# Optimization experiments

Measured on AMD Instinct MI355X. Metric: run time of the kernel, lower is better.

The kernel has to match this reference:

```python
import jax, jax.numpy as jnp
import numpy as np
import math

# Model dims (from VisionMamba defaults)
D = 768        # embed_dim
DI = 1536      # d_inner = 2*D
N = 16         # d_state
R = 48         # dt_rank = ceil(D/16)
K = 4          # d_conv
DEPTH = 24
B = 4
H, W, P, CIN = 1280, 960, 64, 3
GH, GW = H // P, W // P
NPATCH = GH * GW           # 300
L = NPATCH + 1             # 301 with cls token
POS = NPATCH // 2          # middle cls token position = 150
NCLS = 1000
EPS = 1e-5


def setup_inputs() -> dict:
    key = jax.random.key(0)
    c = [0]
    def nk():
        c[0] += 1
        return jax.random.fold_in(key, c[0])
    def rn(shape, s=0.02):
        return jax.random.normal(nk(), shape, jnp.float32) * s
    inp = {}
    inp['img'] = jax.random.normal(nk(), (B, CIN, H, W), jnp.float32)
    inp['patch_w'] = rn((D, CIN, P, P))
    inp['patch_b'] = jnp.zeros((D,), jnp.float32)
    inp['cls_token'] = rn((1, 1, D))
    inp['pos_embed'] = rn((1, L, D))
    inp['norm_w'] = jnp.ones((DEPTH, D), jnp.float32)
    inp['in_proj_w'] = rn((DEPTH, 2 * DI, D))
    for s in ('f', 'b'):
        inp[f'conv_{s}_w'] = rn((DEPTH, DI, K), 0.1)
        inp[f'conv_{s}_b'] = jnp.zeros((DEPTH, DI), jnp.float32)
        inp[f'xproj_{s}_w'] = rn((DEPTH, R + 2 * N, DI))
        inp[f'dt_{s}_w'] = rn((DEPTH, DI, R), 0.1)
        dtv = jnp.exp(jax.random.uniform(nk(), (DEPTH, DI), jnp.float32,
                                         math.log(1e-3), math.log(1e-1)))
        inp[f'dt_{s}_b'] = jnp.log(jnp.expm1(dtv))  # softplus-inverse init
        inp[f'A_{s}_log'] = jnp.broadcast_to(
            jnp.log(jnp.arange(1, N + 1, dtype=jnp.float32)), (DEPTH, DI, N)) + 0.0
        inp[f'D_{s}'] = jnp.ones((DEPTH, DI), jnp.float32)
    inp['out_proj_w'] = rn((DEPTH, D, DI))
    inp['norm_f_w'] = jnp.ones((D,), jnp.float32)
    inp['head_w'] = rn((NCLS, D))
    inp['head_b'] = jnp.zeros((NCLS,), jnp.float32)
    return inp


def _rms(x, w):
    return x * jax.lax.rsqrt(jnp.mean(x * x, axis=-1, keepdims=True) + EPS) * w


def _silu(x):
    return x * jax.nn.sigmoid(x)


def _cconv(x, w, b):
    # depthwise causal conv1d, x: [B,L,DI], w: [DI,K]
    Lx = x.shape[1]
    xp = jnp.pad(x, ((0, 0), (K - 1, 0), (0, 0)))
    return sum(xp[:, k:k + Lx, :] * w[:, k] for k in range(K)) + b


def _ssm(xc, z, xproj_w, dt_w, dt_b, A_log, Dp):
    # selective scan; xc, z: [B,L,DI]
    dbl = jnp.einsum('bld,ed->ble', xc, xproj_w)        # [B,L,R+2N]
    dt_r, Bm, Cm = dbl[..., :R], dbl[..., R:R + N], dbl[..., R + N:]
    dt = jax.nn.softplus(jnp.einsum('blr,dr->bld', dt_r, dt_w) + dt_b)
    A = -jnp.exp(A_log)                                 # [DI,N]
    dA = jnp.exp(dt[..., None] * A)                     # [B,L,DI,N]
    dBu = (dt * xc)[..., None] * Bm[:, :, None, :]      # [B,L,DI,N]
    def step(h, ab):
        a, bu = ab
        h = a * h + bu
        return h, h
    h0 = jnp.zeros((dA.shape[0], DI, N), dA.dtype)
    _, hs = jax.lax.scan(step, h0, (jnp.swapaxes(dA, 0, 1), jnp.swapaxes(dBu, 0, 1)))
    y = jnp.einsum('lbdn,bln->bld', hs, Cm) + xc * Dp
    return y * _silu(z)


def _mixer(h, p):
    (in_w, cfw, cfb, xfw, dtfw, dtfb, Afl, Df,
     cbw, cbb, xbw, dtbw, dtbb, Abl, Db, ow) = p
    xz = jnp.einsum('bld,ed->ble', h, in_w)
    x, z = xz[..., :DI], xz[..., DI:]
    yf = _ssm(_silu(_cconv(x, cfw, cfb)), z, xfw, dtfw, dtfb, Afl, Df)
    xr, zr = x[:, ::-1], z[:, ::-1]
    yb = _ssm(_silu(_cconv(xr, cbw, cbb)), zr, xbw, dtbw, dtbb, Abl, Db)
    y = (yf + yb[:, ::-1]) * 0.5   # bimamba v2 with if_divide_out=True
    return jnp.einsum('ble,de->bld', y, ow)


def _forward(img, patch_w, patch_b, cls_token, pos_embed, norm_w, in_proj_w,
             conv_f_w, conv_f_b, xproj_f_w, dt_f_w, dt_f_b, A_f_log, D_f,
             conv_b_w, conv_b_b, xproj_b_w, dt_b_w, dt_b_b, A_b_log, D_b,
             out_proj_w, norm_f_w, head_w, head_b):
    Bn = img.shape[0]
    # non-overlapping conv patch embed (kernel == stride == 64)
    x = img.reshape(Bn, CIN, GH, P, GW, P)
    x = jnp.einsum('bcipjq,dcpq->bijd', x, patch_w).reshape(Bn, NPATCH, D) + patch_b
    cls = jnp.broadcast_to(cls_token, (Bn, 1, D))
    x = jnp.concatenate([x[:, :POS], cls, x[:, POS:]], axis=1) + pos_embed
    layer_params = (norm_w, in_proj_w, conv_f_w, conv_f_b, xproj_f_w, dt_f_w,
                    dt_f_b, A_f_log, D_f, conv_b_w, conv_b_b, xproj_b_w,
                    dt_b_w, dt_b_b, A_b_log, D_b, out_proj_w)
    def layer(carry, p):
        h, res = carry
        res = res + h                # fused add-norm: Add -> RMSNorm -> Mixer
        hn = _rms(res, p[0])
        h2 = _mixer(hn, p[1:])
        return (h2, res), None
    (h, res), _ = jax.lax.scan(layer, (x, jnp.zeros_like(x)), layer_params)
    out = _rms(res + h, norm_f_w)
    return jnp.einsum('bd,cd->bc', out[:, POS], head_w) + head_b


def reference(img, patch_w, patch_b, cls_token, pos_embed, norm_w, in_proj_w,
              conv_f_w, conv_f_b, xproj_f_w, dt_f_w, dt_f_b, A_f_log, D_f,
              conv_b_w, conv_b_b, xproj_b_w, dt_b_w, dt_b_b, A_b_log, D_b,
              out_proj_w, norm_f_w, head_w, head_b):
    return _forward(img, patch_w, patch_b, cls_token, pos_embed, norm_w,
                    in_proj_w, conv_f_w, conv_f_b, xproj_f_w, dt_f_w, dt_f_b,
                    A_f_log, D_f, conv_b_w, conv_b_b, xproj_b_w, dt_b_w,
                    dt_b_b, A_b_log, D_b, out_proj_w, norm_f_w, head_w, head_b)
```

## Files before the change

kernel.cpp:

```cpp
#include <hip/hip_runtime.h>
#include <hip/hip_bf16.h>
#include <math.h>

#define B_ 4
#define L_ 301
#define D_ 768
#define DI_ 1536
#define NP_ 300
#define POS_ 150
#define M_ 1204
#define SCHUNK 64

typedef __bf16 bf16;
typedef __attribute__((ext_vector_type(8))) __bf16 bf16x8;
typedef __attribute__((ext_vector_type(4))) float floatx4;

__device__ __forceinline__ float siluf(float x) { return x / (1.f + __expf(-x)); }
__device__ __forceinline__ float softplusf(float x) { return x > 20.f ? x : log1pf(__expf(x)); }

__global__ __launch_bounds__(256) void gemm_mfma(
    const bf16* __restrict__ A0, const bf16* __restrict__ A1, int lda,
    const float* __restrict__ W0, const float* __restrict__ W1, int ldw,
    const float* __restrict__ bias0, const float* __restrict__ bias1,
    float* __restrict__ C0, float* __restrict__ C1,
    bf16* __restrict__ Cb0, bf16* __restrict__ Cb1, int ldc,
    int M, int Nw, int Kw, int Ksteps, int act)
{
    const int zz = blockIdx.z;
    const bf16* A = zz ? A1 : A0;
    const float* W = zz ? W1 : W0;
    const float* bias = zz ? bias1 : bias0;
    float* C = zz ? C1 : C0;
    bf16* Cb = zz ? Cb1 : Cb0;

    __shared__ bf16 As[128 * 32];
    __shared__ bf16 Ws[128 * 32];
    const int t = threadIdx.x;
    const int bm = blockIdx.y * 128;
    const int bn = blockIdx.x * 128;
    const int lane = t & 63;
    const int wid = t >> 6;
    const int wr = wid >> 1, wc = wid & 1;
    const int ar = t >> 2;
    const int ac = (t & 3) * 8;

    const bool fullNK = ((Nw & 127) == 0) && ((Kw & 31) == 0);

    floatx4 acc[4][4] = {};

    for (int ks = 0; ks < Ksteps; ks++) {
        const int k0 = ks * 32;
#pragma unroll
        for (int c2 = 0; c2 < 2; c2++) {
            int r = ar + c2 * 64;
            int gm = bm + r; if (gm >= M) gm = M - 1;
            const bf16* gp = A + (size_t)gm * lda + k0 + ac;
            __builtin_amdgcn_global_load_lds(
                (const __attribute__((address_space(1))) void*)gp,
                (__attribute__((address_space(3))) void*)(As + r * 32 + ac),
                16, 0, 0);
        }
#pragma unroll
        for (int c2 = 0; c2 < 2; c2++) {
            int r = ar + c2 * 64;
            int gn = bn + r;
            float vv[8];
            if (fullNK) {
                const floatx4* wp4 = (const floatx4*)(W + (size_t)gn * ldw + k0 + ac);
                floatx4 a4 = wp4[0], b4 = wp4[1];
#pragma unroll
                for (int e = 0; e < 4; e++) { vv[e] = a4[e]; vv[e + 4] = b4[e]; }
            } else {
                const float* wp = W + (size_t)gn * ldw + k0 + ac;
#pragma unroll
                for (int e = 0; e < 8; e++) {
                    int kk = k0 + ac + e;
                    vv[e] = (gn < Nw && kk < Kw) ? wp[e] : 0.f;
                }
            }
            bf16x8 pk;
#pragma unroll
            for (int e = 0; e < 8; e++) pk[e] = (bf16)vv[e];
            *(bf16x8*)(Ws + r * 32 + ac) = pk;
        }
        __syncthreads();
        const int ra = wr * 64 + (lane & 15);
        const int rb = wc * 64 + (lane & 15);
        const int kb = (lane >> 4) * 8;
        bf16x8 af[4], bfm[4];
#pragma unroll
        for (int i = 0; i < 4; i++)
            af[i] = *(const bf16x8*)(As + (ra + i * 16) * 32 + kb);
#pragma unroll
        for (int j = 0; j < 4; j++)
            bfm[j] = *(const bf16x8*)(Ws + (rb + j * 16) * 32 + kb);
#pragma unroll
        for (int i = 0; i < 4; i++)
#pragma unroll
            for (int j = 0; j < 4; j++)
                acc[i][j] = __builtin_amdgcn_mfma_f32_16x16x32_bf16(af[i], bfm[j], acc[i][j], 0, 0, 0);
        __syncthreads();
    }
#pragma unroll
    for (int i = 0; i < 4; i++) {
#pragma unroll
        for (int j = 0; j < 4; j++) {
            int n = bn + wc * 64 + j * 16 + (lane & 15);
            if (n >= Nw) continue;
            float bv = (act >= 1) ? bias[n] : 0.f;
#pragma unroll
            for (int r = 0; r < 4; r++) {
                int m = bm + wr * 64 + i * 16 + (lane >> 4) * 4 + r;
                if (m >= M) continue;
                float v = acc[i][j][r] + bv;
                if (act == 2) v = softplusf(v);
                C[(size_t)m * ldc + n] = v;
                if (Cb) Cb[(size_t)m * ldc + n] = (bf16)v;
            }
        }
    }
}

__global__ __launch_bounds__(256) void gemm_mfma_sk(
    const bf16* __restrict__ A0, const bf16* __restrict__ A1, int lda,
    const float* __restrict__ W0, const float* __restrict__ W1, int ldw,
    float* __restrict__ Cp, size_t chunkStride, int ldc,
    int M, int Nw, int KstepsPer, int SK)
{
    const int z = blockIdx.z;
    const int dir = z / SK;
    const int chunk = z % SK;
    const bf16* A = dir ? A1 : A0;
    const float* W = dir ? W1 : W0;
    float* C = Cp + (size_t)z * chunkStride;

    __shared__ bf16 As[128 * 32];
    __shared__ bf16 Ws[128 * 32];
    const int t = threadIdx.x;
    const int bm = blockIdx.y * 128;
    const int bn = blockIdx.x * 128;
    const int lane = t & 63;
    const int wid = t >> 6;
    const int wr = wid >> 1, wc = wid & 1;
    const int ar = t >> 2;
    const int ac = (t & 3) * 8;

    floatx4 acc[4][4] = {};

    for (int ks = 0; ks < KstepsPer; ks++) {
        const int k0 = (chunk * KstepsPer + ks) * 32;
#pragma unroll
        for (int c2 = 0; c2 < 2; c2++) {
            int r = ar + c2 * 64;
            int gm = bm + r; if (gm >= M) gm = M - 1;
            const bf16* gp = A + (size_t)gm * lda + k0 + ac;
            __builtin_amdgcn_global_load_lds(
                (const __attribute__((address_space(1))) void*)gp,
                (__attribute__((address_space(3))) void*)(As + r * 32 + ac),
                16, 0, 0);
        }
#pragma unroll
        for (int c2 = 0; c2 < 2; c2++) {
            int r = ar + c2 * 64;
            int gn = bn + r;
            bf16x8 pk;
            if (gn < Nw) {
                const floatx4* wp4 = (const floatx4*)(W + (size_t)gn * ldw + k0 + ac);
                floatx4 a4 = wp4[0], b4 = wp4[1];
#pragma unroll
                for (int e = 0; e < 4; e++) { pk[e] = (bf16)a4[e]; pk[e + 4] = (bf16)b4[e]; }
            } else {
#pragma unroll
                for (int e = 0; e < 8; e++) pk[e] = (bf16)0.f;
            }
            *(bf16x8*)(Ws + r * 32 + ac) = pk;
        }
        __syncthreads();
        const int ra = wr * 64 + (lane & 15);
        const int rb = wc * 64 + (lane & 15);
        const int kb = (lane >> 4) * 8;
        bf16x8 af[4], bfm[4];
#pragma unroll
        for (int i = 0; i < 4; i++)
            af[i] = *(const bf16x8*)(As + (ra + i * 16) * 32 + kb);
#pragma unroll
        for (int j = 0; j < 4; j++)
            bfm[j] = *(const bf16x8*)(Ws + (rb + j * 16) * 32 + kb);
#pragma unroll
        for (int i = 0; i < 4; i++)
#pragma unroll
            for (int j = 0; j < 4; j++)
                acc[i][j] = __builtin_amdgcn_mfma_f32_16x16x32_bf16(af[i], bfm[j], acc[i][j], 0, 0, 0);
        __syncthreads();
    }
#pragma unroll
    for (int i = 0; i < 4; i++) {
#pragma unroll
        for (int j = 0; j < 4; j++) {
            int n = bn + wc * 64 + j * 16 + (lane & 15);
            if (n >= Nw) continue;
#pragma unroll
            for (int r = 0; r < 4; r++) {
                int m = bm + wr * 64 + i * 16 + (lane >> 4) * 4 + r;
                if (m >= M) continue;
                C[(size_t)m * ldc + n] = acc[i][j][r];
            }
        }
    }
}

__global__ __launch_bounds__(256) void gemm_mfma_avg_sk(
    const bf16* __restrict__ Af, const bf16* __restrict__ Ab, int lda,
    const float* __restrict__ W, int ldw,
    float* __restrict__ Cp, size_t chunkStride, int ldc,
    int M, int Nw, int KstepsPer, int SK)
{
    const int chunk = blockIdx.z;
    float* C = Cp + (size_t)chunk * chunkStride;

    __shared__ bf16 As[128 * 32];
    __shared__ bf16 Ws[128 * 32];
    const int t = threadIdx.x;
    const int bm = blockIdx.y * 128;
    const int bn = blockIdx.x * 128;
    const int lane = t & 63;
    const int wid = t >> 6;
    const int wr = wid >> 1, wc = wid & 1;
    const int ar = t >> 2;
    const int ac = (t & 3) * 8;

    floatx4 acc[4][4] = {};

    for (int ks = 0; ks < KstepsPer; ks++) {
        const int k0 = (chunk * KstepsPer + ks) * 32;
#pragma unroll
        for (int c2 = 0; c2 < 2; c2++) {
            int r = ar + c2 * 64;
            int gm = bm + r; if (gm >= M) gm = M - 1;
            bf16x8 a8 = *(const bf16x8*)(Af + (size_t)gm * lda + k0 + ac);
            bf16x8 b8 = *(const bf16x8*)(Ab + (size_t)gm * lda + k0 + ac);
            bf16x8 pk;
#pragma unroll
            for (int e = 0; e < 8; e++)
                pk[e] = (bf16)(0.5f * ((float)a8[e] + (float)b8[e]));
            *(bf16x8*)(As + r * 32 + ac) = pk;
        }
#pragma unroll
        for (int c2 = 0; c2 < 2; c2++) {
            int r = ar + c2 * 64;
            int gn = bn + r;
            const floatx4* wp4 = (const floatx4*)(W + (size_t)gn * ldw + k0 + ac);
            floatx4 a4 = wp4[0], b4 = wp4[1];
            bf16x8 pk;
#pragma unroll
            for (int e = 0; e < 4; e++) { pk[e] = (bf16)a4[e]; pk[e + 4] = (bf16)b4[e]; }
            *(bf16x8*)(Ws + r * 32 + ac) = pk;
        }
        __syncthreads();
        const int ra = wr * 64 + (lane & 15);
        const int rb = wc * 64 + (lane & 15);
        const int kb = (lane >> 4) * 8;
        bf16x8 af[4], bfm[4];
#pragma unroll
        for (int i = 0; i < 4; i++)
            af[i] = *(const bf16x8*)(As + (ra + i * 16) * 32 + kb);
#pragma unroll
        for (int j = 0; j < 4; j++)
            bfm[j] = *(const bf16x8*)(Ws + (rb + j * 16) * 32 + kb);
#pragma unroll
        for (int i = 0; i < 4; i++)
#pragma unroll
            for (int j = 0; j < 4; j++)
                acc[i][j] = __builtin_amdgcn_mfma_f32_16x16x32_bf16(af[i], bfm[j], acc[i][j], 0, 0, 0);
        __syncthreads();
    }
#pragma unroll
    for (int i = 0; i < 4; i++) {
#pragma unroll
        for (int j = 0; j < 4; j++) {
            int n = bn + wc * 64 + j * 16 + (lane & 15);
            if (n >= Nw) continue;
#pragma unroll
            for (int r = 0; r < 4; r++) {
                int m = bm + wr * 64 + i * 16 + (lane >> 4) * 4 + r;
                if (m >= M) continue;
                C[(size_t)m * ldc + n] = acc[i][j][r];
            }
        }
    }
}

__global__ void reduce_sk2(const float* __restrict__ Cp, size_t chunkStride, int SK,
                           const float* __restrict__ bias0,
                           float* __restrict__ C0, float* __restrict__ C1,
                           bf16* __restrict__ Cb0, bf16* __restrict__ Cb1,
                           int total, int ldn, int act)
{
    const int dir = blockIdx.y;
    const float* P = Cp + (size_t)dir * SK * chunkStride;
    float* C = dir ? C1 : C0;
    bf16* Cb = dir ? Cb1 : Cb0;
    int idx = blockIdx.x * 256 + threadIdx.x;
    if (idx >= total) return;
    float s = 0.f;
    for (int c = 0; c < SK; c++) s += P[(size_t)c * chunkStride + idx];
    if (act >= 1) s += bias0[idx % ldn];
    if (act == 2) s = softplusf(s);
    C[idx] = s;
    if (Cb) Cb[idx] = (bf16)s;
}

__global__ __launch_bounds__(256) void gemm_patch_mfma(
    const float* __restrict__ img, const float* __restrict__ W,
    float* __restrict__ Cp)
{
    __shared__ bf16 As[128 * 32];
    __shared__ bf16 Ws[128 * 32];
    const int t = threadIdx.x;
    const int bm = blockIdx.y * 128;
    const int bn = blockIdx.x * 128;
    const int chunk = blockIdx.z;
    const int lane = t & 63;
    const int wid = t >> 6;
    const int wr = wid >> 1, wc = wid & 1;
    const int ar = t >> 2;
    const int ac = (t & 3) * 8;
    const int M = 1200, ldw = 12288, ldc = 768;
    float* C = Cp + (size_t)chunk * M * ldc;

    const float* abase[2];
#pragma unroll
    for (int c2 = 0; c2 < 2; c2++) {
        int gm = bm + ar + c2 * 64; if (gm >= M) gm = M - 1;
        int b = gm / 300, rem = gm % 300;
        int gi = rem / 15, gj = rem % 15;
        abase[c2] = img + ((size_t)(b * 3) * 1280 + gi * 64) * 960 + gj * 64;
    }

    floatx4 acc[4][4] = {};

    for (int ks = 0; ks < 48; ks++) {
        const int k0 = (chunk * 48 + ks) * 32;
        const int k = k0 + ac;
        const int q = k & 63, p = (k >> 6) & 63, c = k >> 12;
#pragma unroll
        for (int c2 = 0; c2 < 2; c2++) {
            int r = ar + c2 * 64;
            const float* ip = abase[c2] + ((size_t)c * 1280 + p) * 960 + q;
            const floatx4* ip4 = (const floatx4*)ip;
            floatx4 a4 = ip4[0], b4 = ip4[1];
            bf16x8 pk;
#pragma unroll
            for (int e = 0; e < 4; e++) { pk[e] = (bf16)a4[e]; pk[e + 4] = (bf16)b4[e]; }
            *(bf16x8*)(As + r * 32 + ac) = pk;
        }
#pragma unroll
        for (int c2 = 0; c2 < 2; c2++) {
            int r = ar + c2 * 64;
            int gn = bn + r;
            const floatx4* wp4 = (const floatx4*)(W + (size_t)gn * ldw + k);
            floatx4 a4 = wp4[0], b4 = wp4[1];
            bf16x8 pk;
#pragma unroll
            for (int e = 0; e < 4; e++) { pk[e] = (bf16)a4[e]; pk[e + 4] = (bf16)b4[e]; }
            *(bf16x8*)(Ws + r * 32 + ac) = pk;
        }
        __syncthreads();
        const int ra = wr * 64 + (lane & 15);
        const int rb = wc * 64 + (lane & 15);
        const int kb = (lane >> 4) * 8;
        bf16x8 af[4], bfm[4];
#pragma unroll
        for (int i = 0; i < 4; i++)
            af[i] = *(const bf16x8*)(As + (ra + i * 16) * 32 + kb);
#pragma unroll
        for (int j = 0; j < 4; j++)
            bfm[j] = *(const bf16x8*)(Ws + (rb + j * 16) * 32 + kb);
#pragma unroll
        for (int i = 0; i < 4; i++)
#pragma unroll
            for (int j = 0; j < 4; j++)
                acc[i][j] = __builtin_amdgcn_mfma_f32_16x16x32_bf16(af[i], bfm[j], acc[i][j], 0, 0, 0);
        __syncthreads();
    }
#pragma unroll
    for (int i = 0; i < 4; i++) {
#pragma unroll
        for (int j = 0; j < 4; j++) {
            int n = bn + wc * 64 + j * 16 + (lane & 15);
#pragma unroll
            for (int r = 0; r < 4; r++) {
                int m = bm + wr * 64 + i * 16 + (lane >> 4) * 4 + r;
                if (m >= M) continue;
                C[(size_t)m * ldc + n] = acc[i][j][r];
            }
        }
    }
}

__global__ void gemm_bt(const float* __restrict__ A, int lda,
                        const float* __restrict__ W, int ldw,
                        const float* __restrict__ bias,
                        float* __restrict__ C, int ldc,
                        int M, int N, int K, int act) {
    __shared__ float As[16][68];
    __shared__ float Ws[16][68];
    const int tid = threadIdx.x;
    const int bm = blockIdx.y * 64;
    const int bn = blockIdx.x * 64;
    const int tx = tid & 15, ty = tid >> 4;
    float acc[4][4] = {};
    const int lk = tid & 15;
    const int lm = tid >> 4;
    for (int k0 = 0; k0 < K; k0 += 16) {
        const int ak = k0 + lk;
#pragma unroll
        for (int i = 0; i < 4; i++) {
            int m = bm + lm + i * 16;
            float v = 0.f;
            if (m < M && ak < K) v = A[(long)m * lda + ak];
            As[lk][lm + i * 16] = v;
        }
#pragma unroll
        for (int i = 0; i < 4; i++) {
            int n = bn + lm + i * 16;
            float v = 0.f;
            if (n < N && ak < K) v = W[(long)n * ldw + ak];
            Ws[lk][lm + i * 16] = v;
        }
        __syncthreads();
#pragma unroll
        for (int kk = 0; kk < 16; kk++) {
            float a[4], w[4];
#pragma unroll
            for (int i = 0; i < 4; i++) a[i] = As[kk][ty * 4 + i];
#pragma unroll
            for (int j = 0; j < 4; j++) w[j] = Ws[kk][tx * 4 + j];
#pragma unroll
            for (int i = 0; i < 4; i++)
#pragma unroll
                for (int j = 0; j < 4; j++) acc[i][j] += a[i] * w[j];
        }
        __syncthreads();
    }
#pragma unroll
    for (int i = 0; i < 4; i++) {
        int m = bm + ty * 4 + i;
        if (m >= M) continue;
#pragma unroll
        for (int j = 0; j < 4; j++) {
            int n = bn + tx * 4 + j;
            if (n >= N) continue;
            float v = acc[i][j];
            if (act >= 1) v += bias[n];
            C[(long)m * ldc + n] = v;
        }
    }
}

__global__ void assemble(const float* __restrict__ xt, const float* __restrict__ cls,
                         const float* __restrict__ pos, float* __restrict__ x,
                         float* __restrict__ res) {
    int idx = blockIdx.x * 256 + threadIdx.x;
    if (idx >= B_ * L_ * D_) return;
    int d = idx % D_;
    int l = (idx / D_) % L_;
    int b = idx / (D_ * L_);
    float v;
    if (l == POS_) {
        v = cls[d];
    } else {
        int p = (l < POS_) ? l : l - 1;
        v = xt[((long)b * NP_ + p) * D_ + d];
    }
    x[idx] = v + pos[l * D_ + d];
    res[idx] = 0.f;
}

__global__ void add_rms(float* __restrict__ res, const float* __restrict__ h,
                        const float* __restrict__ w, bf16* __restrict__ hn) {
    int row = blockIdx.x;
    float* rr = res + (long)row * D_;
    const float* hr = h + (long)row * D_;
    float v[3];
    float ss = 0.f;
#pragma unroll
    for (int i = 0; i < 3; i++) {
        int d = threadIdx.x + i * 256;
        float t = rr[d] + hr[d];
        v[i] = t;
        ss += t * t;
    }
#pragma unroll
    for (int off = 1; off < 64; off <<= 1) ss += __shfl_xor(ss, off);
    __shared__ float red[4];
    __shared__ float inv;
    if ((threadIdx.x & 63) == 0) red[threadIdx.x >> 6] = ss;
    __syncthreads();
    if (threadIdx.x == 0) {
        float s = red[0] + red[1] + red[2] + red[3];
        inv = rsqrtf(s / (float)D_ + 1e-5f);
    }
    __syncthreads();
    float iv = inv;
#pragma unroll
    for (int i = 0; i < 3; i++) {
        int d = threadIdx.x + i * 256;
        rr[d] = v[i];
        hn[(long)row * D_ + d] = (bf16)(v[i] * iv * w[d]);
    }
}

__global__ void conv_silu2(const float* __restrict__ xz,
                           const float* __restrict__ wf, const float* __restrict__ bf_,
                           const float* __restrict__ wb, const float* __restrict__ bb_,
                           float* __restrict__ of, bf16* __restrict__ ofb,
                           float* __restrict__ ob, bf16* __restrict__ obb) {
    int idx = blockIdx.x * 256 + threadIdx.x;
    if (idx >= B_ * L_ * DI_) return;
    const int rev = blockIdx.y;
    const float* w = rev ? wb : wf;
    const float* bias = rev ? bb_ : bf_;
    float* out = rev ? ob : of;
    bf16* outb = rev ? obb : ofb;
    int d = idx % DI_;
    int l = (idx / DI_) % L_;
    int b = idx / (DI_ * L_);
    float acc = bias[d];
#pragma unroll
    for (int k = 0; k < 4; k++) {
        int ls = l - 3 + k;
        if (ls < 0) continue;
        int lsrc = rev ? (L_ - 1 - ls) : ls;
        acc += xz[((long)(b * L_ + lsrc)) * (2 * DI_) + d] * w[d * 4 + k];
    }
    float v = siluf(acc);
    out[idx] = v;
    outb[idx] = (bf16)v;
}

__global__ __launch_bounds__(256) void ssm_scan2(
    const float* __restrict__ xcF, const float* __restrict__ dtF, const float* __restrict__ dblF,
    const float* __restrict__ xcB, const float* __restrict__ dtB, const float* __restrict__ dblB,
    const float* __restrict__ xz,
    const float* __restrict__ AF, const float* __restrict__ DF,
    const float* __restrict__ AB, const float* __restrict__ DB,
    bf16* __restrict__ yF, bf16* __restrict__ yB)
{
    const int rev = blockIdx.y;
    const float* xc = rev ? xcB : xcF;
    const float* dt = rev ? dtB : dtF;
    const float* dbl = rev ? dblB : dblF;
    const float* Alog = rev ? AB : AF;
    const float* Dp = rev ? DB : DF;
    bf16* yout = rev ? yB : yF;

    const int t = threadIdx.x;
    const int n = t & 15;
    const int g = t >> 4;
    const int gb = blockIdx.x;
    const int b = gb / (DI_ / 16);
    const int d0 = (gb % (DI_ / 16)) * 16;
    const int d = d0 + g;

    __shared__ float dt_s[SCHUNK][16];
    __shared__ float xc_s[SCHUNK][16];
    __shared__ float z_s[SCHUNK][16];
    __shared__ float bm_s[SCHUNK][16];
    __shared__ float cm_s[SCHUNK][16];
    __shared__ float y_s[SCHUNK][16];

    const float a = -__expf(Alog[(size_t)d * 16 + n]);
    const float Dv = Dp[d];
    float h = 0.f;
    const size_t rowbase = (size_t)b * L_;

    for (int c0 = 0; c0 < L_; c0 += SCHUNK) {
        const int Tc = min(SCHUNK, L_ - c0);
        for (int i = t; i < Tc * 16; i += 256) {
            int ll = i >> 4, dd = i & 15;
            int l = c0 + ll;
            size_t r = (rowbase + l) * DI_ + d0 + dd;
            dt_s[ll][dd] = dt[r];
            xc_s[ll][dd] = xc[r];
            int lz = rev ? (L_ - 1 - l) : l;
            z_s[ll][dd] = xz[(rowbase + lz) * (2 * DI_) + DI_ + d0 + dd];
            bm_s[ll][dd] = dbl[(rowbase + l) * 80 + 48 + dd];
            cm_s[ll][dd] = dbl[(rowbase + l) * 80 + 64 + dd];
        }
        __syncthreads();
#pragma unroll 4
        for (int ll = 0; ll < Tc; ll++) {
            float dtv = dt_s[ll][g];
            float xcv = xc_s[ll][g];
            float bm = bm_s[ll][n];
            float cm = cm_s[ll][n];
            h = __expf(dtv * a) * h + dtv * xcv * bm;
            float cc = h * cm;
            cc += __shfl_xor(cc, 1);
            cc += __shfl_xor(cc, 2);
            cc += __shfl_xor(cc, 4);
            cc += __shfl_xor(cc, 8);
            if (n == 0) {
                float yv = (cc + xcv * Dv) * siluf(z_s[ll][g]);
                y_s[ll][g] = yv;
            }
        }
        __syncthreads();
        for (int i = t; i < Tc * 16; i += 256) {
            int ll = i >> 4, dd = i & 15;
            int l = c0 + ll;
            int lo = rev ? (L_ - 1 - l) : l;
            yout[(rowbase + lo) * DI_ + d0 + dd] = (bf16)y_s[ll][dd];
        }
        __syncthreads();
    }
}

__global__ void final_rms(const float* __restrict__ res, const float* __restrict__ h,
                          const float* __restrict__ w, float* __restrict__ out) {
    int b = blockIdx.x;
    long base = ((long)b * L_ + POS_) * D_;
    float v[3];
    float ss = 0.f;
#pragma unroll
    for (int i = 0; i < 3; i++) {
        int d = threadIdx.x + i * 256;
        float t = res[base + d] + h[base + d];
        v[i] = t;
        ss += t * t;
    }
#pragma unroll
    for (int off = 1; off < 64; off <<= 1) ss += __shfl_xor(ss, off);
    __shared__ float red[4];
    __shared__ float inv;
    if ((threadIdx.x & 63) == 0) red[threadIdx.x >> 6] = ss;
    __syncthreads();
    if (threadIdx.x == 0) {
        float s = red[0] + red[1] + red[2] + red[3];
        inv = rsqrtf(s / (float)D_ + 1e-5f);
    }
    __syncthreads();
    float iv = inv;
#pragma unroll
    for (int i = 0; i < 3; i++) {
        int d = threadIdx.x + i * 256;
        out[b * D_ + d] = v[i] * iv * w[d];
    }
}

extern "C" void kernel_launch(void* const* d_in, const int* in_sizes, int n_in,
                              void* d_out, int out_size, void* d_ws, size_t ws_size,
                              hipStream_t stream) {
    const float* img = (const float*)d_in[0];
    const float* patch_w = (const float*)d_in[1];
    const float* patch_b = (const float*)d_in[2];
    const float* cls_token = (const float*)d_in[3];
    const float* pos_embed = (const float*)d_in[4];
    const float* norm_w = (const float*)d_in[5];
    const float* in_proj_w = (const float*)d_in[6];
    const float* conv_f_w = (const float*)d_in[7];
    const float* conv_f_b = (const float*)d_in[8];
    const float* xproj_f_w = (const float*)d_in[9];
    const float* dt_f_w = (const float*)d_in[10];
    const float* dt_f_b = (const float*)d_in[11];
    const float* A_f_log = (const float*)d_in[12];
    const float* D_f = (const float*)d_in[13];
    const float* conv_b_w = (const float*)d_in[14];
    const float* conv_b_b = (const float*)d_in[15];
    const float* xproj_b_w = (const float*)d_in[16];
    const float* dt_b_w = (const float*)d_in[17];
    const float* dt_b_b = (const float*)d_in[18];
    const float* A_b_log = (const float*)d_in[19];
    const float* D_b = (const float*)d_in[20];
    const float* out_proj_w = (const float*)d_in[21];
    const float* norm_f_w = (const float*)d_in[22];
    const float* head_w = (const float*)d_in[23];
    const float* head_b = (const float*)d_in[24];

    char* p8 = (char*)d_ws;
    auto alloc = [&](size_t nb) { char* r = p8; p8 += (nb + 255) & ~(size_t)255; return r; };
    float* x    = (float*)alloc((size_t)M_ * D_ * 4);
    float* res  = (float*)alloc((size_t)M_ * D_ * 4);
    bf16*  hnb  = (bf16*) alloc((size_t)M_ * D_ * 2);
    float* xz   = (float*)alloc((size_t)M_ * 2 * DI_ * 4);
    float* xcf  = (float*)alloc((size_t)M_ * DI_ * 4);
    float* xcb  = (float*)alloc((size_t)M_ * DI_ * 4);
    bf16*  xcfb = (bf16*) alloc((size_t)M_ * DI_ * 2);
    bf16*  xcbb = (bf16*) alloc((size_t)M_ * DI_ * 2);
    float* dtf  = (float*)alloc((size_t)M_ * DI_ * 4);
    float* dtb  = (float*)alloc((size_t)M_ * DI_ * 4);
    bf16*  yfb  = (bf16*) alloc((size_t)M_ * DI_ * 2);
    bf16*  ybb  = (bf16*) alloc((size_t)M_ * DI_ * 2);
    float* dblf = (float*)alloc((size_t)M_ * 80 * 4);
    float* dblb = (float*)alloc((size_t)M_ * 80 * 4);
    bf16*  dblfb= (bf16*) alloc((size_t)M_ * 80 * 2);
    bf16*  dblbb= (bf16*) alloc((size_t)M_ * 80 * 2);
    float* clsv = (float*)alloc((size_t)B_ * D_ * 4);
    float* xtmp = dtf;

    float* patchP = xz;
    float* xprojP = dtf;
    float* outP   = dtf;

    gemm_patch_mfma<<<dim3(6, 10, 8), 256, 0, stream>>>(img, patch_w, patchP);
    reduce_sk2<<<dim3((1200 * 768 + 255) / 256, 1), 256, 0, stream>>>(
        patchP, (size_t)1200 * 768, 8, patch_b, xtmp, nullptr, nullptr, nullptr,
        1200 * 768, 768, 1);
    assemble<<<(B_ * L_ * D_ + 255) / 256, 256, 0, stream>>>(xtmp, cls_token, pos_embed, x, res);

    for (int layer = 0; layer < 24; layer++) {
        const float* ipw = in_proj_w + (size_t)layer * 2 * DI_ * D_;
        const float* cfw = conv_f_w + (size_t)layer * DI_ * 4;
        const float* cfb = conv_f_b + (size_t)layer * DI_;
        const float* xfw = xproj_f_w + (size_t)layer * 80 * DI_;
        const float* dfw = dt_f_w + (size_t)layer * DI_ * 48;
        const float* dfb = dt_f_b + (size_t)layer * DI_;
        const float* afl = A_f_log + (size_t)layer * DI_ * 16;
        const float* df = D_f + (size_t)layer * DI_;
        const float* cbw = conv_b_w + (size_t)layer * DI_ * 4;
        const float* cbb = conv_b_b + (size_t)layer * DI_;
        const float* xbw = xproj_b_w + (size_t)layer * 80 * DI_;
        const float* dbw = dt_b_w + (size_t)layer * DI_ * 48;
        const float* dbb = dt_b_b + (size_t)layer * DI_;
        const float* abl = A_b_log + (size_t)layer * DI_ * 16;
        const float* db = D_b + (size_t)layer * DI_;
        const float* opw = out_proj_w + (size_t)layer * D_ * DI_;
        const float* nw = norm_w + (size_t)layer * D_;

        add_rms<<<M_, 256, 0, stream>>>(res, x, nw, hnb);
        gemm_mfma<<<dim3(24, 10, 1), 256, 0, stream>>>(
            hnb, hnb, D_, ipw, ipw, D_, nullptr, nullptr,
            xz, xz, nullptr, nullptr, 2 * DI_, M_, 2 * DI_, D_, 24, 0);
        conv_silu2<<<dim3((B_ * L_ * DI_ + 255) / 256, 2), 256, 0, stream>>>(
            xz, cfw, cfb, cbw, cbb, xcf, xcfb, xcb, xcbb);
        gemm_mfma_sk<<<dim3(1, 10, 16), 256, 0, stream>>>(
            xcfb, xcbb, DI_, xfw, xbw, DI_,
            xprojP, (size_t)M_ * 80, 80, M_, 80, 6, 8);
        reduce_sk2<<<dim3((M_ * 80 + 255) / 256, 2), 256, 0, stream>>>(
            xprojP, (size_t)M_ * 80, 8, nullptr,
            dblf, dblb, dblfb, dblbb, M_ * 80, 80, 0);
        gemm_mfma<<<dim3(12, 10, 2), 256, 0, stream>>>(
            dblfb, dblbb, 80, dfw, dbw, 48, dfb, dbb,
            dtf, dtb, nullptr, nullptr, DI_, M_, DI_, 48, 2, 2);
        ssm_scan2<<<dim3(384, 2), 256, 0, stream>>>(
            xcf, dtf, dblf, xcb, dtb, dblb, xz, afl, df, abl, db, yfb, ybb);
        gemm_mfma_avg_sk<<<dim3(6, 10, 4), 256, 0, stream>>>(
            yfb, ybb, DI_, opw, DI_,
            outP, (size_t)M_ * D_, D_, M_, D_, 12, 4);
        reduce_sk2<<<dim3((M_ * D_ + 255) / 256, 1), 256, 0, stream>>>(
            outP, (size_t)M_ * D_, 4, nullptr,
            x, nullptr, nullptr, nullptr, M_ * D_, D_, 0);
    }

    final_rms<<<B_, 256, 0, stream>>>(res, x, norm_f_w, clsv);
    gemm_bt<<<dim3(16, 1), 256, 0, stream>>>(clsv, D_, head_w, D_, head_b,
                                             (float*)d_out, 1000, B_, 1000, D_, 1);
}
```

Baseline: 7.338 ms.

## Split selective scan into chunked two-pass scan across sequence chunks

Replaces the single sequential SSM scan kernel with a two-pass chunked scan. The first pass computes each chunk's end state and cumulative decay product. The second pass seeds each chunk with the combined prefix state and then runs the full output computation. This multiplies the number of blocks by the chunk count to expose more parallelism along the sequence, at the cost of an extra kernel launch, re-reading the inputs twice, and small scratch buffers.

```diff
diff --git a/kernel.cpp b/kernel.cpp
--- a/kernel.cpp
+++ b/kernel.cpp
@@ -9,7 +9,8 @@
 #define NP_ 300
 #define POS_ 150
 #define M_ 1204
-#define SCHUNK 64
+#define NC_ 5
+#define CL_ 64
 
 typedef __bf16 bf16;
 typedef __attribute__((ext_vector_type(8))) __bf16 bf16x8;
@@ -539,21 +540,18 @@
     outb[idx] = (bf16)v;
 }
 
-__global__ __launch_bounds__(256) void ssm_scan2(
+__global__ __launch_bounds__(256) void ssm_p1(
     const float* __restrict__ xcF, const float* __restrict__ dtF, const float* __restrict__ dblF,
     const float* __restrict__ xcB, const float* __restrict__ dtB, const float* __restrict__ dblB,
-    const float* __restrict__ xz,
-    const float* __restrict__ AF, const float* __restrict__ DF,
-    const float* __restrict__ AB, const float* __restrict__ DB,
-    bf16* __restrict__ yF, bf16* __restrict__ yB)
+    const float* __restrict__ AF, const float* __restrict__ AB,
+    float* __restrict__ Hend, float* __restrict__ Aprod)
 {
     const int rev = blockIdx.y;
+    const int c = blockIdx.z;
     const float* xc = rev ? xcB : xcF;
     const float* dt = rev ? dtB : dtF;
     const float* dbl = rev ? dblB : dblF;
     const float* Alog = rev ? AB : AF;
-    const float* Dp = rev ? DB : DF;
-    bf16* yout = rev ? yB : yF;
 
     const int t = threadIdx.x;
     const int n = t & 15;
@@ -563,57 +561,120 @@
     const int d0 = (gb % (DI_ / 16)) * 16;
     const int d = d0 + g;
 
-    __shared__ float dt_s[SCHUNK][16];
-    __shared__ float xc_s[SCHUNK][16];
-    __shared__ float z_s[SCHUNK][16];
-    __shared__ float bm_s[SCHUNK][16];
-    __shared__ float cm_s[SCHUNK][16];
-    __shared__ float y_s[SCHUNK][16];
+    __shared__ float dt_s[CL_][16];
+    __shared__ float xc_s[CL_][16];
+    __shared__ float bm_s[CL_][16];
+
+    const float a = -__expf(Alog[(size_t)d * 16 + n]);
+    const size_t rowbase = (size_t)b * L_;
+    const int c0 = c * CL_;
+
+    for (int i = t; i < CL_ * 16; i += 256) {
+        int ll = i >> 4, dd = i & 15;
+        int l = c0 + ll;
+        size_t r = (rowbase + l) * DI_ + d0 + dd;
+        dt_s[ll][dd] = dt[r];
+        xc_s[ll][dd] = xc[r];
+        bm_s[ll][dd] = dbl[(rowbase + l) * 80 + 48 + dd];
+    }
+    __syncthreads();
+
+    float h = 0.f, sdt = 0.f;
+#pragma unroll 4
+    for (int ll = 0; ll < CL_; ll++) {
+        float dtv = dt_s[ll][g];
+        float xcv = xc_s[ll][g];
+        float bm = bm_s[ll][n];
+        h = __expf(dtv * a) * h + dtv * xcv * bm;
+        sdt += dtv;
+    }
+    size_t o = (((size_t)rev * (NC_ - 1) + c) * 384 + gb) * 256 + t;
+    Hend[o] = h;
+    Aprod[o] = __expf(a * sdt);
+}
+
+__global__ __launch_bounds__(256) void ssm_p2(
+    const float* __restrict__ xcF, const float* __restrict__ dtF, const float* __restrict__ dblF,
+    const float* __restrict__ xcB, const float* __restrict__ dtB, const float* __restrict__ dblB,
+    const float* __restrict__ xz,
+    const float* __restrict__ AF, const float* __restrict__ DF,
+    const float* __restrict__ AB, const float* __restrict__ DB,
+    const float* __restrict__ Hend, const float* __restrict__ Aprod,
+    bf16* __restrict__ yF, bf16* __restrict__ yB)
+{
+    const int rev = blockIdx.y;
+    const int c = blockIdx.z;
+    const float* xc = rev ? xcB : xcF;
+    const float* dt = rev ? dtB : dtF;
+    const float* dbl = rev ? dblB : dblF;
+    const float* Alog = rev ? AB : AF;
+    const float* Dp = rev ? DB : DF;
+    bf16* yout = rev ? yB : yF;
+
+    const int t = threadIdx.x;
+    const int n = t & 15;
+    const int g = t >> 4;
+    const int gb = blockIdx.x;
+    const int b = gb / (DI_ / 16);
+    const int d0 = (gb % (DI_ / 16)) * 16;
+    const int d = d0 + g;
+
+    __shared__ float dt_s[CL_][16];
+    __shared__ float xc_s[CL_][16];
+    __shared__ float z_s[CL_][16];
+    __shared__ float bm_s[CL_][16];
+    __shared__ float cm_s[CL_][16];
+    __shared__ float y_s[CL_][16];
 
     const float a = -__expf(Alog[(size_t)d * 16 + n]);
     const float Dv = Dp[d];
+    const size_t rowbase = (size_t)b * L_;
+    const int c0 = c * CL_;
+    const int Tc = min(CL_, L_ - c0);
+
+    for (int i = t; i < Tc * 16; i += 256) {
+        int ll = i >> 4, dd = i & 15;
+        int l = c0 + ll;
+        size_t r = (rowbase + l) * DI_ + d0 + dd;
+        dt_s[ll][dd] = dt[r];
+        xc_s[ll][dd] = xc[r];
+        int lz = rev ? (L_ - 1 - l) : l;
+        z_s[ll][dd] = xz[(rowbase + lz) * (2 * DI_) + DI_ + d0 + dd];
+        bm_s[ll][dd] = dbl[(rowbase + l) * 80 + 48 + dd];
+        cm_s[ll][dd] = dbl[(rowbase + l) * 80 + 64 + dd];
+    }
+
     float h = 0.f;
-    const size_t rowbase = (size_t)b * L_;
-
-    for (int c0 = 0; c0 < L_; c0 += SCHUNK) {
-        const int Tc = min(SCHUNK, L_ - c0);
-        for (int i = t; i < Tc * 16; i += 256) {
-            int ll = i >> 4, dd = i & 15;
-            int l = c0 + ll;
-            size_t r = (rowbase + l) * DI_ + d0 + dd;
-            dt_s[ll][dd] = dt[r];
-            xc_s[ll][dd] = xc[r];
-            int lz = rev ? (L_ - 1 - l) : l;
-            z_s[ll][dd] = xz[(rowbase + lz) * (2 * DI_) + DI_ + d0 + dd];
-            bm_s[ll][dd] = dbl[(rowbase + l) * 80 + 48 + dd];
-            cm_s[ll][dd] = dbl[(rowbase + l) * 80 + 64 + dd];
-        }
-        __syncthreads();
+    for (int j = 0; j < c; j++) {
+        size_t o = (((size_t)rev * (NC_ - 1) + j) * 384 + gb) * 256 + t;
+        h = Aprod[o] * h + Hend[o];
+    }
+    __syncthreads();
+
 #pragma unroll 4
-        for (int ll = 0; ll < Tc; ll++) {
-            float dtv = dt_s[ll][g];
-            float xcv = xc_s[ll][g];
-            float bm = bm_s[ll][n];
-            float cm = cm_s[ll][n];
-            h = __expf(dtv * a) * h + dtv * xcv * bm;
-            float cc = h * cm;
-            cc += __shfl_xor(cc, 1);
-            cc += __shfl_xor(cc, 2);
-            cc += __shfl_xor(cc, 4);
-            cc += __shfl_xor(cc, 8);
-            if (n == 0) {
-                float yv = (cc + xcv * Dv) * siluf(z_s[ll][g]);
-                y_s[ll][g] = yv;
-            }
-        }
-        __syncthreads();
-        for (int i = t; i < Tc * 16; i += 256) {
-            int ll = i >> 4, dd = i & 15;
-            int l = c0 + ll;
-            int lo = rev ? (L_ - 1 - l) : l;
-            yout[(rowbase + lo) * DI_ + d0 + dd] = (bf16)y_s[ll][dd];
-        }
-        __syncthreads();
+    for (int ll = 0; ll < Tc; ll++) {
+        float dtv = dt_s[ll][g];
+        float xcv = xc_s[ll][g];
+        float bm = bm_s[ll][n];
+        float cm = cm_s[ll][n];
+        h = __expf(dtv * a) * h + dtv * xcv * bm;
+        float cc = h * cm;
+        cc += __shfl_xor(cc, 1);
+        cc += __shfl_xor(cc, 2);
+        cc += __shfl_xor(cc, 4);
+        cc += __shfl_xor(cc, 8);
+        if (n == 0) {
+            float yv = (cc + xcv * Dv) * siluf(z_s[ll][g]);
+            y_s[ll][g] = yv;
+        }
+    }
+    __syncthreads();
+
+    for (int i = t; i < Tc * 16; i += 256) {
+        int ll = i >> 4, dd = i & 15;
+        int l = c0 + ll;
+        int lo = rev ? (L_ - 1 - l) : l;
+        yout[(rowbase + lo) * DI_ + d0 + dd] = (bf16)y_s[ll][dd];
     }
 }
 
@@ -697,6 +758,8 @@
     bf16*  dblfb= (bf16*) alloc((size_t)M_ * 80 * 2);
     bf16*  dblbb= (bf16*) alloc((size_t)M_ * 80 * 2);
     float* clsv = (float*)alloc((size_t)B_ * D_ * 4);
+    float* hend = (float*)alloc((size_t)2 * (NC_ - 1) * 384 * 256 * 4);
+    float* aprd = (float*)alloc((size_t)2 * (NC_ - 1) * 384 * 256 * 4);
     float* xtmp = dtf;
 
     float* patchP = xz;
@@ -743,8 +806,11 @@
         gemm_mfma<<<dim3(12, 10, 2), 256, 0, stream>>>(
             dblfb, dblbb, 80, dfw, dbw, 48, dfb, dbb,
             dtf, dtb, nullptr, nullptr, DI_, M_, DI_, 48, 2, 2);
-        ssm_scan2<<<dim3(384, 2), 256, 0, stream>>>(
-            xcf, dtf, dblf, xcb, dtb, dblb, xz, afl, df, abl, db, yfb, ybb);
+        ssm_p1<<<dim3(384, 2, NC_ - 1), 256, 0, stream>>>(
+            xcf, dtf, dblf, xcb, dtb, dblb, afl, abl, hend, aprd);
+        ssm_p2<<<dim3(384, 2, NC_), 256, 0, stream>>>(
+            xcf, dtf, dblf, xcb, dtb, dblb, xz, afl, df, abl, db,
+            hend, aprd, yfb, ybb);
         gemm_mfma_avg_sk<<<dim3(6, 10, 4), 256, 0, stream>>>(
             yfb, ybb, DI_, opw, DI_,
             outP, (size_t)M_ * D_, D_, M_, D_, 12, 4);
```

Measured after the change: 6.487 ms. -11.6%, faster.
